# Optimization experiments

Hardware: AMD Instinct MI355X
Metric: run time of the kernel (lower is better)

Reference implementation:

```python
import jax, jax.numpy as jnp
import numpy as np

B, T, V, C, NB = 8, 2048, 1024, 128, 32


def setup_inputs() -> dict:
    key = jax.random.key(0)
    ks = jax.random.split(key, 6)
    x = jax.random.normal(ks[0], (B, T, V), jnp.float32)
    basis = jax.random.normal(ks[1], (V, 2 * NB), jnp.float32)
    q_coeffs = jax.random.normal(ks[2], (C, 2 * NB), jnp.float32) * 0.02
    k_coeffs = jax.random.normal(ks[3], (C, 2 * NB), jnp.float32) * 0.02
    v_coeffs = jax.random.normal(ks[4], (C, 2 * NB), jnp.float32) * 0.02
    o_coeffs = jax.random.normal(ks[5], (C, 2 * NB), jnp.float32) * 0.02
    decay = jnp.float32(0.95)
    out_scale = jnp.float32(0.1)
    return {"x": x, "basis": basis, "q_coeffs": q_coeffs, "k_coeffs": k_coeffs,
            "v_coeffs": v_coeffs, "o_coeffs": o_coeffs, "decay": decay, "out_scale": out_scale}


def reference(x, basis, q_coeffs, k_coeffs, v_coeffs, o_coeffs, decay, out_scale):
    # Fourier-parameterized projections: (V, C); softmax over vocab dim for q/k/v
    q_w = jax.nn.softmax(basis @ q_coeffs.T, axis=0)
    k_w = jax.nn.softmax(basis @ k_coeffs.T, axis=0)
    v_w = jax.nn.softmax(basis @ v_coeffs.T, axis=0)
    o_w = basis @ o_coeffs.T  # (V, C), no softmax

    q = x @ q_w  # (B, T, C)
    k = x @ k_w
    v = x @ v_w
    d = jax.nn.sigmoid(decay)

    M0 = jnp.zeros((x.shape[0], q_w.shape[1], q_w.shape[1]), x.dtype)  # (B, C, C)

    def step(M, qkv_t):
        q_t, k_t, v_t = qkv_t  # each (B, C)
        retrieved = jnp.einsum('bc,bcd->bd', q_t, M)  # read BEFORE write (as in torch loop)
        M_new = d * M + jnp.einsum('bc,bd->bcd', k_t, v_t)
        return M_new, retrieved

    qT = jnp.swapaxes(q, 0, 1)  # (T, B, C)
    kT = jnp.swapaxes(k, 0, 1)
    vT = jnp.swapaxes(v, 0, 1)
    _, rs = jax.lax.scan(step, M0, (qT, kT, vT))  # rs: (T, B, C)
    retrieved = jnp.swapaxes(rs, 0, 1)  # (B, T, C)
    return (retrieved @ o_w.T) * out_scale  # (B, T, V)
```

## Files before the change

### kernel.cpp

```cpp
#include <hip/hip_runtime.h>
#include <math.h>

#define B_   8
#define T_   2048
#define V_   1024
#define C_   128
#define NB2  64
#define L_   32
#define NC_  64

typedef _Float16 f16_t;
typedef f16_t f16x8 __attribute__((ext_vector_type(8)));
typedef float f32x4 __attribute__((ext_vector_type(4)));

__device__ __forceinline__ float sigmoidf_(float x){ return 1.0f/(1.0f+expf(-x)); }

__device__ __forceinline__ void gload_lds16(const void* g, void* l){
  __builtin_amdgcn_global_load_lds(
      (const __attribute__((address_space(1))) uint32_t*)g,
      (__attribute__((address_space(3))) uint32_t*)l, 16, 0, 0);
}

__global__ __launch_bounds__(256) void weights_kernel(
    const float* __restrict__ basis,
    const float* __restrict__ qc, const float* __restrict__ kc,
    const float* __restrict__ vc, const float* __restrict__ oc,
    f16_t* __restrict__ Wo, f16_t* __restrict__ Wt)
{
  int blk  = blockIdx.x;
  int proj = blk >> 7;
  int c    = blk & 127;
  const float* coeffs = (proj==0)?qc : (proj==1)?kc : (proj==2)?vc : oc;

  __shared__ float coef[NB2];
  __shared__ float red[256];
  int tid = threadIdx.x;
  if (tid < NB2) coef[tid] = coeffs[c*NB2 + tid];
  __syncthreads();

  float l[4];
  for (int i=0;i<4;i++){
    int v = tid + i*256;
    const float4* bp = (const float4*)(basis + (size_t)v*NB2);
    float s = 0.f;
    #pragma unroll
    for (int f=0; f<NB2/4; f++){
      float4 b4 = bp[f];
      s += b4.x*coef[f*4+0] + b4.y*coef[f*4+1] + b4.z*coef[f*4+2] + b4.w*coef[f*4+3];
    }
    l[i] = s;
  }
  if (proj == 3){
    for (int i=0;i<4;i++){ int v = tid+i*256; Wo[(size_t)v*C_ + c] = (f16_t)l[i]; }
    return;
  }
  float mx = fmaxf(fmaxf(l[0],l[1]), fmaxf(l[2],l[3]));
  red[tid] = mx; __syncthreads();
  for (int s=128; s>0; s>>=1){ if (tid<s) red[tid] = fmaxf(red[tid], red[tid+s]); __syncthreads(); }
  mx = red[0]; __syncthreads();
  float sum = 0.f;
  for (int i=0;i<4;i++) sum += expf(l[i]-mx);
  red[tid] = sum; __syncthreads();
  for (int s=128; s>0; s>>=1){ if (tid<s) red[tid] += red[tid+s]; __syncthreads(); }
  float inv = 1.0f/red[0];
  f16_t* tp = Wt + ((size_t)proj*C_ + c)*V_;
  for (int i=0;i<4;i++){
    int v = tid+i*256;
    tp[v] = (f16_t)(expf(l[i]-mx)*inv);
  }
}

#define BM 64
#define BN 128
#define BK 64
#define PADK 72
#define NF_  384
#define NT_PROJ (V_/BK)

__global__ __launch_bounds__(512, 1) void proj_fused_kernel(
    const float* __restrict__ x,
    const f16_t* __restrict__ Wt,
    float* __restrict__ out)
{
  const int M = B_*T_;
  int m0 = blockIdx.x * BM;

  __shared__ __align__(16) f16_t As[BM][PADK];
  __shared__ __align__(16) f16_t Bsh[NF_*BK];

  int tid  = threadIdx.x;
  int lane = tid & 63;
  int w    = tid >> 6;
  int wm   = (w >> 2) * 32;
  int wn   = (w & 3) * 96;
  int lr   = lane & 15;
  int lg   = lane >> 4;

  const float* xbase = x + (size_t)m0*V_;

  f32x4 acc[2][6] = {};

  for (int kt = 0; kt < NT_PROJ; kt++){
    #pragma unroll
    for (int i=0;i<6;i++){
      int ci = i*512 + tid;
      int r  = ci >> 3, ch = ci & 7;
      const f16_t* src = Wt + (size_t)r*V_ + kt*BK + ((ch ^ (r&7))<<3);
      gload_lds16(src, &Bsh[ci*8]);
    }
    #pragma unroll
    for (int i=0;i<2;i++){
      int ci = i*512 + tid;
      int row = ci >> 4, q = ci & 15;
      float4 xv = *(const float4*)(xbase + (size_t)row*V_ + kt*BK + q*4);
      union { f16_t h[4]; ushort4 u; } hh;
      hh.h[0]=(f16_t)xv.x; hh.h[1]=(f16_t)xv.y; hh.h[2]=(f16_t)xv.z; hh.h[3]=(f16_t)xv.w;
      *(ushort4*)&As[row][q*4] = hh.u;
    }
    __syncthreads();

    #pragma unroll
    for (int kh=0; kh<2; kh++){
      f16x8 a[2];
      #pragma unroll
      for (int mt=0; mt<2; mt++)
        a[mt] = *(f16x8*)&As[wm + mt*16 + lr][kh*32 + lg*8];
      #pragma unroll
      for (int nt=0; nt<6; nt++){
        int n  = wn + nt*16 + lr;
        int c0 = kh*4 + lg;
        f16x8 b = *(f16x8*)&Bsh[n*BK + ((c0 ^ (n&7))<<3)];
        #pragma unroll
        for (int mt=0; mt<2; mt++)
          acc[mt][nt] = __builtin_amdgcn_mfma_f32_16x16x32_f16(a[mt], b, acc[mt][nt], 0,0,0);
      }
    }
    __syncthreads();
  }

  #pragma unroll
  for (int mt=0; mt<2; mt++)
    #pragma unroll
    for (int nt=0; nt<6; nt++){
      int n   = wn + nt*16 + lr;
      int p   = n >> 7;
      int col = n & 127;
      float* op = out + (size_t)p*M*C_;
      #pragma unroll
      for (int r=0; r<4; r++){
        int row = m0 + wm + mt*16 + lg*4 + r;
        op[(size_t)row*C_ + col] = acc[mt][nt][r];
      }
    }
}

__global__ __launch_bounds__(256) void kvsum_kernel(
    const float* __restrict__ k, const float* __restrict__ v,
    const float* __restrict__ dptr, float* __restrict__ kv)
{
  int ci = blockIdx.x, b = blockIdx.y;
  float d = sigmoidf_(dptr[0]);
  __shared__ float ks[L_][132];
  __shared__ float vs[L_][132];
  int tid = threadIdx.x;
  const float* kp = k + ((size_t)b*T_ + ci*L_)*C_;
  const float* vp = v + ((size_t)b*T_ + ci*L_)*C_;
  #pragma unroll
  for (int i=0;i<4;i++){
    int idx = tid + i*256;
    int j = idx >> 5, c4 = idx & 31;
    float w = powf(d, (float)(L_-1-j));
    float4 k4 = *(const float4*)(kp + (size_t)j*C_ + c4*4);
    k4.x*=w; k4.y*=w; k4.z*=w; k4.w*=w;
    *(float4*)&ks[j][c4*4] = k4;
    *(float4*)&vs[j][c4*4] = *(const float4*)(vp + (size_t)j*C_ + c4*4);
  }
  __syncthreads();
  int tc = tid >> 4, td = tid & 15;
  float acc[8][8] = {};
  for (int j=0;j<L_;j++){
    float kr[8], vr[8];
    *(float4*)&kr[0] = *(float4*)&ks[j][tc*8];
    *(float4*)&kr[4] = *(float4*)&ks[j][tc*8+4];
    *(float4*)&vr[0] = *(float4*)&vs[j][td*8];
    *(float4*)&vr[4] = *(float4*)&vs[j][td*8+4];
    #pragma unroll
    for (int a=0;a<8;a++)
      #pragma unroll
      for (int bb=0;bb<8;bb++) acc[a][bb] += kr[a]*vr[bb];
  }
  float* op = kv + ((size_t)b*NC_ + ci)*C_*C_;
  for (int a=0;a<8;a++)
    for (int b4=0;b4<2;b4++)
      *(float4*)(op + (size_t)(tc*8+a)*C_ + td*8 + b4*4) =
        make_float4(acc[a][b4*4],acc[a][b4*4+1],acc[a][b4*4+2],acc[a][b4*4+3]);
}

__global__ __launch_bounds__(256) void scan_kernel(
    float* __restrict__ kv, const float* __restrict__ dptr)
{
  int idx = blockIdx.x*256 + threadIdx.x;
  int b = idx >> 14, e = idx & 16383;
  float d  = sigmoidf_(dptr[0]);
  float dL = powf(d, (float)L_);
  float* p = kv + (size_t)b*NC_*C_*C_ + e;
  float m = 0.f;
  for (int i=0;i<NC_;i++){
    float s = p[(size_t)i*C_*C_];
    p[(size_t)i*C_*C_] = m;
    m = dL*m + s;
  }
}

__global__ __launch_bounds__(256) void intra_kernel(
    const float* __restrict__ q, const float* __restrict__ k,
    const float* __restrict__ v, const float* __restrict__ Minit,
    const float* __restrict__ dptr,
    f16_t* __restrict__ ret)
{
  int ci = blockIdx.x, b = blockIdx.y;
  int tid = threadIdx.x;
  float d = sigmoidf_(dptr[0]);
  __shared__ float qs[L_][132];
  __shared__ float kvs[L_][132];
  __shared__ float ps[L_][33];
  __shared__ float dpow[L_+1];
  if (tid <= L_) dpow[tid] = powf(d, (float)tid);

  const float* qp = q + ((size_t)b*T_ + ci*L_)*C_;
  const float* kp = k + ((size_t)b*T_ + ci*L_)*C_;
  const float* vp = v + ((size_t)b*T_ + ci*L_)*C_;
  #pragma unroll
  for (int i=0;i<4;i++){
    int idx = tid + i*256;
    int j = idx >> 5, c4 = idx & 31;
    *(float4*)&qs[j][c4*4]  = *(const float4*)(qp + (size_t)j*C_ + c4*4);
    *(float4*)&kvs[j][c4*4] = *(const float4*)(kp + (size_t)j*C_ + c4*4);
  }
  __syncthreads();

  {
    int tr = tid >> 4, tj = tid & 15;
    float s[2][2] = {};
    for (int c4=0;c4<32;c4++){
      float4 q4[2], k4[2];
      #pragma unroll
      for (int i=0;i<2;i++) q4[i] = *(float4*)&qs[tr*2+i][c4*4];
      #pragma unroll
      for (int i=0;i<2;i++) k4[i] = *(float4*)&kvs[tj*2+i][c4*4];
      #pragma unroll
      for (int a=0;a<2;a++)
        #pragma unroll
        for (int bb=0;bb<2;bb++)
          s[a][bb] += q4[a].x*k4[bb].x + q4[a].y*k4[bb].y + q4[a].z*k4[bb].z + q4[a].w*k4[bb].w;
    }
    #pragma unroll
    for (int a=0;a<2;a++)
      #pragma unroll
      for (int bb=0;bb<2;bb++){
        int r = tr*2+a, j = tj*2+bb;
        ps[r][j] = (j < r) ? s[a][bb]*dpow[r-1-j] : 0.f;
      }
  }
  __syncthreads();
  #pragma unroll
  for (int i=0;i<4;i++){
    int idx = tid + i*256;
    int j = idx >> 5, c4 = idx & 31;
    *(float4*)&kvs[j][c4*4] = *(const float4*)(vp + (size_t)j*C_ + c4*4);
  }
  __syncthreads();

  int tx = tid & 31, ty = tid >> 5;
  float acc[4][4] = {};
  const float* Mp = Minit + ((size_t)b*NC_ + ci)*C_*C_;
  for (int c=0;c<C_;c++){
    float4 m4 = *(const float4*)(Mp + (size_t)c*C_ + tx*4);
    #pragma unroll
    for (int r=0;r<4;r++){
      float qv = qs[ty*4+r][c];
      acc[r][0] += qv*m4.x; acc[r][1] += qv*m4.y; acc[r][2] += qv*m4.z; acc[r][3] += qv*m4.w;
    }
  }
  #pragma unroll
  for (int r=0;r<4;r++){
    float sc = dpow[ty*4+r];
    #pragma unroll
    for (int j=0;j<4;j++) acc[r][j] *= sc;
  }
  for (int j=0;j<L_;j++){
    float4 v4 = *(float4*)&kvs[j][tx*4];
    #pragma unroll
    for (int r=0;r<4;r++){
      float p = ps[ty*4+r][j];
      acc[r][0] += p*v4.x; acc[r][1] += p*v4.y; acc[r][2] += p*v4.z; acc[r][3] += p*v4.w;
    }
  }
  size_t rbase = ((size_t)b*T_ + ci*L_)*C_;
  for (int r=0;r<4;r++){
    union { f16_t h[4]; ushort4 u; } hh;
    #pragma unroll
    for (int j=0;j<4;j++) hh.h[j] = (f16_t)acc[r][j];
    *(ushort4*)(ret + rbase + (size_t)(ty*4+r)*C_ + tx*4) = hh.u;
  }
}

__global__ __launch_bounds__(256, 2) void out_mfma_kernel(
    const f16_t* __restrict__ A, const f16_t* __restrict__ Bw,
    const float* __restrict__ scl, float* __restrict__ out)
{
  int m0 = blockIdx.x * BM;
  int n0 = blockIdx.y * BN;
  float osc = scl[0];

  __shared__ f16_t As[BM][PADK];
  __shared__ f16_t Bs[BN][PADK];

  int tid  = threadIdx.x;
  int lane = tid & 63;
  int w    = tid >> 6;
  int wm   = (w >> 1) * 32;
  int wn   = (w & 1) * 64;
  int lr   = lane & 15;
  int lg   = lane >> 4;

  f32x4 acc[2][4] = {};

  for (int kt = 0; kt < 2; kt++){
    #pragma unroll
    for (int i=0;i<2;i++){
      int ci = tid + i*256;
      int row = ci >> 3, ch = ci & 7;
      *(uint4*)&As[row][ch*8] = *(const uint4*)(A + (size_t)(m0+row)*C_ + kt*BK + ch*8);
    }
    #pragma unroll
    for (int i=0;i<4;i++){
      int ci = tid + i*256;
      int n = ci >> 3, ch = ci & 7;
      *(uint4*)&Bs[n][ch*8] = *(const uint4*)(Bw + (size_t)(n0+n)*C_ + kt*BK + ch*8);
    }
    __syncthreads();

    #pragma unroll
    for (int kh=0; kh<2; kh++){
      f16x8 a[2];
      #pragma unroll
      for (int mt=0; mt<2; mt++)
        a[mt] = *(f16x8*)&As[wm + mt*16 + lr][kh*32 + lg*8];
      #pragma unroll
      for (int nt=0; nt<4; nt++){
        f16x8 b = *(f16x8*)&Bs[wn + nt*16 + lr][kh*32 + lg*8];
        #pragma unroll
        for (int mt=0; mt<2; mt++)
          acc[mt][nt] = __builtin_amdgcn_mfma_f32_16x16x32_f16(a[mt], b, acc[mt][nt], 0,0,0);
      }
    }
    __syncthreads();
  }

  #pragma unroll
  for (int mt=0; mt<2; mt++)
    #pragma unroll
    for (int nt=0; nt<4; nt++)
      #pragma unroll
      for (int r=0; r<4; r++){
        int row = m0 + wm + mt*16 + lg*4 + r;
        int col = n0 + wn + nt*16 + lr;
        out[(size_t)row*V_ + col] = acc[mt][nt][r] * osc;
      }
}

extern "C" void kernel_launch(void* const* d_in, const int* in_sizes, int n_in,
                              void* d_out, int out_size, void* d_ws, size_t ws_size,
                              hipStream_t stream)
{
  const float* x     = (const float*)d_in[0];
  const float* basis = (const float*)d_in[1];
  const float* qc    = (const float*)d_in[2];
  const float* kc    = (const float*)d_in[3];
  const float* vc    = (const float*)d_in[4];
  const float* oc    = (const float*)d_in[5];
  const float* dptr  = (const float*)d_in[6];
  const float* sptr  = (const float*)d_in[7];
  float* out = (float*)d_out;
  float* ws  = (float*)d_ws;

  const size_t M = (size_t)B_*T_;
  f16_t* Wo  = (f16_t*)ws;
  f16_t* Wt  = (f16_t*)(ws + 65536);
  float* qkv = ws + 262144;
  f16_t* ret = (f16_t*)(ws + 6553600);
  float* kv  = ws + 7602176;

  float* q = qkv;
  float* k = qkv + M*C_;
  float* v = qkv + 2*M*C_;

  hipLaunchKernelGGL(weights_kernel, dim3(512), dim3(256), 0, stream,
                     basis, qc, kc, vc, oc, Wo, Wt);
  hipLaunchKernelGGL(proj_fused_kernel, dim3(256), dim3(512), 0, stream,
                     x, Wt, qkv);
  hipLaunchKernelGGL(kvsum_kernel, dim3(NC_, B_), dim3(256), 0, stream, k, v, dptr, kv);
  hipLaunchKernelGGL(scan_kernel, dim3(512), dim3(256), 0, stream, kv, dptr);
  hipLaunchKernelGGL(intra_kernel, dim3(NC_, B_), dim3(256), 0, stream,
                     q, k, v, kv, dptr, ret);
  hipLaunchKernelGGL(out_mfma_kernel, dim3(256, 8), dim3(256), 0, stream,
                     ret, Wo, sptr, out);
}
```

Measured before the change: 254.4 us.

## Double-buffer chunk state M through LDS with register prefetch in intra kernel

The intra-chunk kernel used to read the 128x128 chunk-initial state M straight from global memory inside the q·M loop, with each of the 8 row groups re-reading the same rows. It now loads M in 32-row slices into registers, stages them in a double-buffered LDS array, and prefetches the next slice while the current one is consumed. It also sets a launch-bounds occupancy hint of 3 and drops one barrier by merging the v load with the M staging sync. The cost is 32KB of extra LDS per block, which may limit occupancy, plus more barriers.

```diff
diff --git a/kernel.cpp b/kernel.cpp
--- a/kernel.cpp
+++ b/kernel.cpp
@@ -212,7 +212,7 @@
   }
 }
 
-__global__ __launch_bounds__(256) void intra_kernel(
+__global__ __launch_bounds__(256, 3) void intra_kernel(
     const float* __restrict__ q, const float* __restrict__ k,
     const float* __restrict__ v, const float* __restrict__ Minit,
     const float* __restrict__ dptr,
@@ -223,6 +223,7 @@
   float d = sigmoidf_(dptr[0]);
   __shared__ float qs[L_][132];
   __shared__ float kvs[L_][132];
+  __shared__ float Ms[2][L_][C_];
   __shared__ float ps[L_][33];
   __shared__ float dpow[L_+1];
   if (tid <= L_) dpow[tid] = powf(d, (float)tid);
@@ -230,6 +231,16 @@
   const float* qp = q + ((size_t)b*T_ + ci*L_)*C_;
   const float* kp = k + ((size_t)b*T_ + ci*L_)*C_;
   const float* vp = v + ((size_t)b*T_ + ci*L_)*C_;
+  const float* Mp = Minit + ((size_t)b*NC_ + ci)*C_*C_;
+
+  int mr0 = tid >> 5;
+  int mc4 = tid & 31;
+
+  float4 mreg[4];
+  #pragma unroll
+  for (int i=0;i<4;i++)
+    mreg[i] = *(const float4*)(Mp + (size_t)(mr0 + i*8)*C_ + mc4*4);
+
   #pragma unroll
   for (int i=0;i<4;i++){
     int idx = tid + i*256;
@@ -262,26 +273,59 @@
         ps[r][j] = (j < r) ? s[a][bb]*dpow[r-1-j] : 0.f;
       }
   }
-  __syncthreads();
+  #pragma unroll
+  for (int i=0;i<4;i++) *(float4*)&Ms[0][mr0 + i*8][mc4*4] = mreg[i];
+  #pragma unroll
+  for (int i=0;i<4;i++)
+    mreg[i] = *(const float4*)(Mp + (size_t)(L_ + mr0 + i*8)*C_ + mc4*4);
+  __syncthreads();
+
   #pragma unroll
   for (int i=0;i<4;i++){
     int idx = tid + i*256;
     int j = idx >> 5, c4 = idx & 31;
     *(float4*)&kvs[j][c4*4] = *(const float4*)(vp + (size_t)j*C_ + c4*4);
   }
-  __syncthreads();
 
   int tx = tid & 31, ty = tid >> 5;
   float acc[4][4] = {};
-  const float* Mp = Minit + ((size_t)b*NC_ + ci)*C_*C_;
-  for (int c=0;c<C_;c++){
-    float4 m4 = *(const float4*)(Mp + (size_t)c*C_ + tx*4);
-    #pragma unroll
-    for (int r=0;r<4;r++){
-      float qv = qs[ty*4+r][c];
-      acc[r][0] += qv*m4.x; acc[r][1] += qv*m4.y; acc[r][2] += qv*m4.z; acc[r][3] += qv*m4.w;
-    }
-  }
+
+#define INTRA_MCHUNK(buf, cc) do { \
+    for (int c=0;c<L_;c++){ \
+      float4 m4 = *(float4*)&Ms[buf][c][tx*4]; \
+      _Pragma("unroll") \
+      for (int r=0;r<4;r++){ \
+        float qv = qs[ty*4+r][(cc)*L_ + c]; \
+        acc[r][0] += qv*m4.x; acc[r][1] += qv*m4.y; \
+        acc[r][2] += qv*m4.z; acc[r][3] += qv*m4.w; \
+      } \
+    } \
+  } while(0)
+
+  INTRA_MCHUNK(0, 0);
+  #pragma unroll
+  for (int i=0;i<4;i++) *(float4*)&Ms[1][mr0 + i*8][mc4*4] = mreg[i];
+  #pragma unroll
+  for (int i=0;i<4;i++)
+    mreg[i] = *(const float4*)(Mp + (size_t)(2*L_ + mr0 + i*8)*C_ + mc4*4);
+  __syncthreads();
+
+  INTRA_MCHUNK(1, 1);
+  #pragma unroll
+  for (int i=0;i<4;i++) *(float4*)&Ms[0][mr0 + i*8][mc4*4] = mreg[i];
+  #pragma unroll
+  for (int i=0;i<4;i++)
+    mreg[i] = *(const float4*)(Mp + (size_t)(3*L_ + mr0 + i*8)*C_ + mc4*4);
+  __syncthreads();
+
+  INTRA_MCHUNK(0, 2);
+  #pragma unroll
+  for (int i=0;i<4;i++) *(float4*)&Ms[1][mr0 + i*8][mc4*4] = mreg[i];
+  __syncthreads();
+
+  INTRA_MCHUNK(1, 3);
+#undef INTRA_MCHUNK
+
   #pragma unroll
   for (int r=0;r<4;r++){
     float sc = dpow[ty*4+r];
```

After: 249.7 us. No clear change (-1.9%).
